# Optimization experiments

Measured on AMD Instinct MI355X. Metric: run time of the kernel, lower is better.

## Reference

```python
import jax, jax.numpy as jnp
import numpy as np


def setup_inputs() -> dict:
    key = jax.random.key(0)
    ks = jax.random.split(key, 11)
    B, T, I, H, O = 64, 256, 1024, 1024, 1024
    s_g = 1.0 / np.sqrt(I + H)  # torch Linear init scale (uniform); use scaled normal
    s_v = 1.0 / np.sqrt(H)
    return {
        "inputs": jax.random.normal(ks[0], (B, T, I), jnp.float32),
        "Wf_w": jax.random.normal(ks[1], (H, I + H), jnp.float32) * s_g,
        "Wf_b": jax.random.normal(ks[2], (H,), jnp.float32) * s_g,
        "Wi_w": jax.random.normal(ks[3], (H, I + H), jnp.float32) * s_g,
        "Wi_b": jax.random.normal(ks[4], (H,), jnp.float32) * s_g,
        "Wc_w": jax.random.normal(ks[5], (H, I + H), jnp.float32) * s_g,
        "Wc_b": jax.random.normal(ks[6], (H,), jnp.float32) * s_g,
        "Wo_w": jax.random.normal(ks[7], (H, I + H), jnp.float32) * s_g,
        "Wo_b": jax.random.normal(ks[8], (H,), jnp.float32) * s_g,
        "V_w": jax.random.normal(ks[9], (O, H), jnp.float32) * s_v,
        "V_b": jax.random.normal(ks[10], (O,), jnp.float32) * s_v,
    }


def reference(inputs, Wf_w, Wf_b, Wi_w, Wi_b, Wc_w, Wc_b, Wo_w, Wo_b, V_w, V_b):
    B, T, I = inputs.shape
    H = Wf_w.shape[0]
    # Fuse the four gate linears into one GEMM (mathematically identical).
    W_all = jnp.concatenate([Wf_w, Wi_w, Wo_w, Wc_w], axis=0)  # (4H, I+H)
    b_all = jnp.concatenate([Wf_b, Wi_b, Wo_b, Wc_b], axis=0)  # (4H,)

    def step(carry, x_t):  # x_t: (B, I)
        c, h = carry
        combined = jnp.concatenate([x_t, h], axis=1)            # (B, I+H)
        gates = combined @ W_all.T + b_all                      # (B, 4H)
        f, i, o, g = jnp.split(gates, 4, axis=1)
        f = jax.nn.sigmoid(f)
        i = jax.nn.sigmoid(i)
        o = jax.nn.sigmoid(o)
        g = jnp.tanh(g)
        c = f * c + i * g
        h = o * jnp.tanh(c)
        return (c, h), None

    c0 = jnp.zeros((B, H), inputs.dtype)
    h0 = jnp.zeros((B, H), inputs.dtype)
    (c, h), _ = jax.lax.scan(step, (c0, h0), jnp.swapaxes(inputs, 0, 1))
    last_out = h @ V_w.T + V_b  # outputs[:, -1, :] only depends on final h
    return (c, h, last_out)
```

## Files before the change

### kernel.cpp

```cpp
#include <hip/hip_runtime.h>
#include <hip/hip_bf16.h>

typedef __bf16 bf16x8 __attribute__((ext_vector_type(8)));
typedef float f32x4 __attribute__((ext_vector_type(4)));
typedef unsigned long long u64;

#define TSTEPS 256
#define NB 64
#define ID 1024
#define HD 1024
#define KD 2048

#define WOFF 0ull
#define VOFF 16777216ull
#define BOFF 18874368ull
#define HMOFF 18890752ull
#define XBOFF 52580352ull

#define SENT 0xFFFFFFFFu

__device__ __forceinline__ unsigned short f2b(float f) {
    unsigned int u = __float_as_uint(f);
    unsigned int r = (u + 0x7fffu + ((u >> 16) & 1u)) >> 16;
    return (unsigned short)r;
}

__device__ __forceinline__ bf16x8 as_frag(uint4 u) {
    union { uint4 u; bf16x8 v; } c; c.u = u; return c.v;
}

__device__ __forceinline__ uint4 ld_b128_cp(const void* p) {
    uint4 r;
    asm volatile("global_load_dwordx4 %0, %1, off sc0 sc1" : "=v"(r) : "v"(p));
    return r;
}
__device__ __forceinline__ uint4 ld_b128(const void* p) {
    uint4 r;
    asm volatile("global_load_dwordx4 %0, %1, off" : "=v"(r) : "v"(p));
    return r;
}

__global__ void cvt_x(const float* __restrict__ in, unsigned short* __restrict__ out) {
    size_t i = ((size_t)blockIdx.x * 256 + threadIdx.x) * 8;
    int t = (int)(i >> 16);
    int b = (int)(i >> 10) & 63;
    int k = (int)i & 1023;
    const float* src = in + ((size_t)b << 18) + ((size_t)t << 10) + k;
    float4 a = *(const float4*)src;
    float4 bb = *(const float4*)(src + 4);
    union { unsigned short h[8]; uint4 u; } o;
    o.h[0] = f2b(a.x); o.h[1] = f2b(a.y); o.h[2] = f2b(a.z); o.h[3] = f2b(a.w);
    o.h[4] = f2b(bb.x); o.h[5] = f2b(bb.y); o.h[6] = f2b(bb.z); o.h[7] = f2b(bb.w);
    *(uint4*)(out + i) = o.u;
}

__global__ void cvt_w(const float* __restrict__ Wf, const float* __restrict__ Wi,
                      const float* __restrict__ Wo, const float* __restrict__ Wc,
                      const float* __restrict__ bf_, const float* __restrict__ bi_,
                      const float* __restrict__ bo_, const float* __restrict__ bc_,
                      unsigned short* __restrict__ Wr, float* __restrict__ bias_r) {
    int idx = blockIdx.x * 256 + threadIdx.x;
    int np = idx >> 8;
    int k  = (idx & 255) * 8;
    int g = np & 3, h = np >> 2;
    const float* W = (g == 0) ? Wf : (g == 1) ? Wi : (g == 2) ? Wo : Wc;
    const float* src = W + (size_t)h * KD + k;
    float4 a = *(const float4*)src;
    float4 b = *(const float4*)(src + 4);
    union { unsigned short h[8]; uint4 u; } o;
    o.h[0] = f2b(a.x); o.h[1] = f2b(a.y); o.h[2] = f2b(a.z); o.h[3] = f2b(a.w);
    o.h[4] = f2b(b.x); o.h[5] = f2b(b.y); o.h[6] = f2b(b.z); o.h[7] = f2b(b.w);
    *(uint4*)(Wr + (size_t)np * KD + k) = o.u;
    if (k == 0) {
        const float* B = (g == 0) ? bf_ : (g == 1) ? bi_ : (g == 2) ? bo_ : bc_;
        bias_r[np] = B[h];
    }
}

__global__ void cvt_v(const float* __restrict__ V, unsigned short* __restrict__ out) {
    size_t i = ((size_t)blockIdx.x * blockDim.x + threadIdx.x) * 8;
    float4 a = *(const float4*)(V + i);
    float4 b = *(const float4*)(V + i + 4);
    union { unsigned short h[8]; uint4 u; } o;
    o.h[0] = f2b(a.x); o.h[1] = f2b(a.y); o.h[2] = f2b(a.z); o.h[3] = f2b(a.w);
    o.h[4] = f2b(b.x); o.h[5] = f2b(b.y); o.h[6] = f2b(b.z); o.h[7] = f2b(b.w);
    *(uint4*)(out + i) = o.u;
}

__global__ void init_h(unsigned short* __restrict__ h0) {
    size_t i = ((size_t)blockIdx.x * blockDim.x + threadIdx.x) * 8;
    uint4 z = {0, 0, 0, 0};
    *(uint4*)(h0 + i) = z;
}

__global__ void init_sent(unsigned short* __restrict__ h1) {
    size_t i = ((size_t)blockIdx.x * blockDim.x + threadIdx.x) * 8;
    uint4 s = {SENT, SENT, SENT, SENT};
    *(uint4*)(h1 + i) = s;
}

__device__ __forceinline__ float sigf(float x) {
    return 1.0f / (1.0f + __expf(-x));
}
__device__ __forceinline__ float tanhfast(float x) {
    return 2.0f / (1.0f + __expf(-2.0f * x)) - 1.0f;
}

__launch_bounds__(512, 1)
__global__ void lstm_core(const unsigned short* __restrict__ xb,
                          const unsigned short* __restrict__ Wr,
                          const float* __restrict__ bias_r,
                          unsigned short* __restrict__ hm,
                          const unsigned short* __restrict__ Vw,
                          const float* __restrict__ Vbias,
                          float* __restrict__ out) {
    __shared__ float gxp[8][64][20];

    const int bid  = blockIdx.x;
    const int tid  = threadIdx.x;
    const int wave = tid >> 6;
    const int lane = tid & 63;
    const int lrow = lane & 15;
    const int kq   = (lane >> 4) << 3;
    const int n0   = bid << 4;
    const int qr   = (lane >> 4) << 2;

    const int ct   = tid - 256;
    const int ob   = (ct >> 2) & 63;
    const int lhc  = ct & 3;
    const int hcol = (bid << 2) + lhc;
    float4 bb = {0, 0, 0, 0};
    if (tid >= 256) bb = *(const float4*)&bias_r[n0 + (lhc << 2)];

    const bool isx = wave < 4;
    const unsigned short* wptr = Wr + (size_t)(n0 + lrow) * KD + (wave << 8) + kq;

    uint4 wfrag[8];
    #pragma unroll
    for (int kk8 = 0; kk8 < 8; ++kk8)
        wfrag[kk8] = ld_b128(wptr + kk8 * 32);
    asm volatile("s_waitcnt vmcnt(0)" ::: "memory");
    __builtin_amdgcn_sched_barrier(0);

    int koff = 0;
    if (!isx) koff = ((wave - 4) << 8) + kq;
    const int xko = (wave << 8) + kq;

    float c_reg = 0.f;
    float hlast = 0.f;

    for (int t = 0; t < TSTEPS; ++t) {
        f32x4 acc[4];
        #pragma unroll
        for (int m = 0; m < 4; ++m) acc[m] = (f32x4){0, 0, 0, 0};

        if (isx) {
            const unsigned short* xt = xb + ((size_t)t << 16);
            #pragma unroll
            for (int kk8 = 0; kk8 < 8; ++kk8)
                #pragma unroll
                for (int m = 0; m < 4; ++m)
                    acc[m] = __builtin_amdgcn_mfma_f32_16x16x32_bf16(
                        *(const bf16x8*)(xt + (size_t)(m * 16 + lrow) * 1024 + xko + kk8 * 32),
                        as_frag(wfrag[kk8]), acc[m], 0, 0, 0);
        } else {
            const unsigned short* hmt = hm + ((size_t)t << 16);
            const int c8b = koff >> 3;
            uint4 hA[4][4], hB[4][4];

            int itA = 0;
            for (;;) {
                #pragma unroll
                for (int j = 0; j < 4; ++j)
                    #pragma unroll
                    for (int m = 0; m < 4; ++m)
                        hA[j][m] = ld_b128_cp(hmt + (size_t)(c8b + j * 4) * 512 + (m * 16 + lrow) * 8);
                asm volatile("s_waitcnt vmcnt(0)" ::: "memory");
                __builtin_amdgcn_sched_barrier(0);
                unsigned int bad = 0;
                #pragma unroll
                for (int j = 0; j < 4; ++j)
                    #pragma unroll
                    for (int m = 0; m < 4; ++m)
                        bad |= (hA[j][m].x == SENT) | (hA[j][m].y == SENT) |
                               (hA[j][m].z == SENT) | (hA[j][m].w == SENT);
                if (__all(bad == 0) || ++itA > (1 << 14)) break;
            }
            __builtin_amdgcn_sched_barrier(0);

            #pragma unroll
            for (int j = 0; j < 4; ++j)
                #pragma unroll
                for (int m = 0; m < 4; ++m)
                    hB[j][m] = ld_b128_cp(hmt + (size_t)(c8b + (j + 4) * 4) * 512 + (m * 16 + lrow) * 8);
            __builtin_amdgcn_sched_barrier(0);

            #pragma unroll
            for (int j = 0; j < 4; ++j)
                #pragma unroll
                for (int m = 0; m < 4; ++m)
                    acc[m] = __builtin_amdgcn_mfma_f32_16x16x32_bf16(as_frag(hA[j][m]),
                                                                     as_frag(wfrag[j]), acc[m], 0, 0, 0);

            int itB = 0;
            for (;;) {
                asm volatile("s_waitcnt vmcnt(0)" ::: "memory");
                __builtin_amdgcn_sched_barrier(0);
                unsigned int bad = 0;
                #pragma unroll
                for (int j = 0; j < 4; ++j)
                    #pragma unroll
                    for (int m = 0; m < 4; ++m)
                        bad |= (hB[j][m].x == SENT) | (hB[j][m].y == SENT) |
                               (hB[j][m].z == SENT) | (hB[j][m].w == SENT);
                if (__all(bad == 0) || ++itB > (1 << 14)) break;
                #pragma unroll
                for (int j = 0; j < 4; ++j)
                    #pragma unroll
                    for (int m = 0; m < 4; ++m)
                        hB[j][m] = ld_b128_cp(hmt + (size_t)(c8b + (j + 4) * 4) * 512 + (m * 16 + lrow) * 8);
            }
            __builtin_amdgcn_sched_barrier(0);

            #pragma unroll
            for (int j = 0; j < 4; ++j)
                #pragma unroll
                for (int m = 0; m < 4; ++m)
                    acc[m] = __builtin_amdgcn_mfma_f32_16x16x32_bf16(as_frag(hB[j][m]),
                                                                     as_frag(wfrag[j + 4]), acc[m], 0, 0, 0);
        }

        #pragma unroll
        for (int m = 0; m < 4; ++m)
            #pragma unroll
            for (int r = 0; r < 4; ++r)
                gxp[wave][m * 16 + qr + r][lrow] = acc[m][r];
        __syncthreads();

        if (tid >= 256) {
            float fpre = bb.x, ipre = bb.y, opre = bb.z, gpre = bb.w;
            #pragma unroll
            for (int w = 0; w < 8; ++w) {
                float4 s = *(const float4*)&gxp[w][ob][lhc << 2];
                fpre += s.x; ipre += s.y; opre += s.z; gpre += s.w;
            }
            float fg = sigf(fpre);
            float ig = sigf(ipre);
            float og = sigf(opre);
            float gg = tanhfast(gpre);
            c_reg = fg * c_reg + ig * gg;
            float hh = og * tanhfast(c_reg);
            if (t == TSTEPS - 1) hlast = hh;

            unsigned int hb = f2b(hh);
            unsigned int p1 = __shfl_down(hb, 1);
            unsigned int p2 = __shfl_down(hb, 2);
            unsigned int p3 = __shfl_down(hb, 3);
            if ((lane & 3) == 0) {
                u64 v = (u64)hb | ((u64)p1 << 16) | ((u64)p2 << 32) | ((u64)p3 << 48);
                unsigned short* dst = hm + ((size_t)(t + 1) << 16)
                                       + (size_t)(bid >> 1) * 512 + (size_t)ob * 8 + ((bid & 1) << 2);
                asm volatile("global_store_dwordx2 %0, %1, off sc0 sc1" :: "v"(dst), "v"(v) : "memory");
            }
        }
        __syncthreads();
    }

    if (tid >= 256) {
        out[(size_t)ob * HD + hcol] = c_reg;
        out[65536 + (size_t)ob * HD + hcol] = hlast;
    }

    if (bid < 64) {
        f32x4 acc[4];
        #pragma unroll
        for (int m = 0; m < 4; ++m) acc[m] = (f32x4){0, 0, 0, 0};
        const int ko2 = (wave << 7) + kq;
        const unsigned short* vp = Vw + (size_t)(n0 + lrow) * HD + ko2;
        const unsigned short* hmt = hm + ((size_t)TSTEPS << 16);
        const int c8b = ko2 >> 3;
        uint4 pw[4], pv[4][4];
        #pragma unroll
        for (int j = 0; j < 4; ++j)
            pw[j] = ld_b128(vp + j * 32);
        int it = 0;
        for (;;) {
            #pragma unroll
            for (int j = 0; j < 4; ++j)
                #pragma unroll
                for (int m = 0; m < 4; ++m)
                    pv[j][m] = ld_b128_cp(hmt + (size_t)(c8b + j * 4) * 512 + (m * 16 + lrow) * 8);
            asm volatile("s_waitcnt vmcnt(0)" ::: "memory");
            __builtin_amdgcn_sched_barrier(0);
            unsigned int bad = 0;
            #pragma unroll
            for (int j = 0; j < 4; ++j)
                #pragma unroll
                for (int m = 0; m < 4; ++m)
                    bad |= (pv[j][m].x == SENT) | (pv[j][m].y == SENT) |
                           (pv[j][m].z == SENT) | (pv[j][m].w == SENT);
            if (__all(bad == 0) || ++it > (1 << 14)) break;
        }
        __builtin_amdgcn_sched_barrier(0);
        #pragma unroll
        for (int j = 0; j < 4; ++j)
            #pragma unroll
            for (int m = 0; m < 4; ++m)
                acc[m] = __builtin_amdgcn_mfma_f32_16x16x32_bf16(as_frag(pv[j][m]),
                                                                 as_frag(pw[j]), acc[m], 0, 0, 0);
        #pragma unroll
        for (int m = 0; m < 4; ++m)
            #pragma unroll
            for (int r = 0; r < 4; ++r)
                gxp[wave][m * 16 + qr + r][lrow] = acc[m][r];
        __syncthreads();
        if (tid >= 256) {
            float4 vb = *(const float4*)&Vbias[n0 + (lhc << 2)];
            float4 res = vb;
            #pragma unroll
            for (int w = 0; w < 8; ++w) {
                float4 s = *(const float4*)&gxp[w][ob][lhc << 2];
                res.x += s.x; res.y += s.y; res.z += s.z; res.w += s.w;
            }
            *(float4*)&out[131072 + (size_t)ob * 1024 + n0 + (lhc << 2)] = res;
        }
    }
}

extern "C" void kernel_launch(void* const* d_in, const int* in_sizes, int n_in,
                              void* d_out, int out_size, void* d_ws, size_t ws_size,
                              hipStream_t stream) {
    const float* x   = (const float*)d_in[0];
    const float* Wf  = (const float*)d_in[1];
    const float* bf_ = (const float*)d_in[2];
    const float* Wi  = (const float*)d_in[3];
    const float* bi_ = (const float*)d_in[4];
    const float* Wc  = (const float*)d_in[5];
    const float* bc_ = (const float*)d_in[6];
    const float* Wo  = (const float*)d_in[7];
    const float* bo_ = (const float*)d_in[8];
    const float* Vw  = (const float*)d_in[9];
    const float* Vb  = (const float*)d_in[10];

    char* ws = (char*)d_ws;
    unsigned short* Wr     = (unsigned short*)(ws + WOFF);
    unsigned short* Vbf    = (unsigned short*)(ws + VOFF);
    float*          bias_r = (float*)(ws + BOFF);
    unsigned short* hm     = (unsigned short*)(ws + HMOFF);
    unsigned short* xbb    = (unsigned short*)(ws + XBOFF);
    float*          outp   = (float*)d_out;

    cvt_x <<<8192, 256, 0, stream>>>(x, xbb);
    cvt_w <<<4096, 256, 0, stream>>>(Wf, Wi, Wo, Wc, bf_, bi_, bo_, bc_, Wr, bias_r);
    cvt_v <<<512, 256, 0, stream>>>(Vw, Vbf);
    init_h<<<32, 256, 0, stream>>>(hm);
    init_sent<<<8192, 256, 0, stream>>>(hm + 65536);

    void* args[] = {&xbb, &Wr, &bias_r, &hm, &Vbf, (void*)&Vb, &outp};
    hipLaunchCooperativeKernel((const void*)lstm_core, dim3(256), dim3(512), args, 0, stream);
}
```

Baseline: 1.462 ms.

## Split waves by batch rows and precompute next-step input projection off critical path

Each of the 4 x-waves now computes the full-K input projection for its 16 batch rows one timestep ahead into a double-buffered shared array. Each of the 4 h-waves handles the full recurrent K for its 16 rows, streaming weights and hidden chunks with double buffering and per-chunk sentinel polling. The same wave then applies the gate nonlinearity, so the 8-wave cross reduction is gone and the t=0 recurrent GEMM and the h0 init kernel are skipped. In exchange, weights are reloaded from global or cache every step instead of being held in registers, which adds memory traffic.

```diff
diff --git a/kernel.cpp b/kernel.cpp
--- a/kernel.cpp
+++ b/kernel.cpp
@@ -87,12 +87,6 @@
     *(uint4*)(out + i) = o.u;
 }
 
-__global__ void init_h(unsigned short* __restrict__ h0) {
-    size_t i = ((size_t)blockIdx.x * blockDim.x + threadIdx.x) * 8;
-    uint4 z = {0, 0, 0, 0};
-    *(uint4*)(h0 + i) = z;
-}
-
 __global__ void init_sent(unsigned short* __restrict__ h1) {
     size_t i = ((size_t)blockIdx.x * blockDim.x + threadIdx.x) * 8;
     uint4 s = {SENT, SENT, SENT, SENT};
@@ -115,6 +109,8 @@
                           const float* __restrict__ Vbias,
                           float* __restrict__ out) {
     __shared__ float gxp[8][64][20];
+    __shared__ float pbx[4][2][16][20];
+    __shared__ float pbh[4][16][20];
 
     const int bid  = blockIdx.x;
     const int tid  = threadIdx.x;
@@ -125,125 +121,117 @@
     const int n0   = bid << 4;
     const int qr   = (lane >> 4) << 2;
 
+    const bool isx = wave < 4;
+    const int w4   = isx ? wave : wave - 4;
+    const int row0 = w4 << 4;
+    const int crow = lane >> 2;
+    const int chc  = lane & 3;
+
+    const unsigned short* wbase = Wr + (size_t)(n0 + lrow) * KD;
+    const float4 bb = *(const float4*)&bias_r[n0 + (chc << 2)];
+
     const int ct   = tid - 256;
     const int ob   = (ct >> 2) & 63;
     const int lhc  = ct & 3;
-    const int hcol = (bid << 2) + lhc;
-    float4 bb = {0, 0, 0, 0};
-    if (tid >= 256) bb = *(const float4*)&bias_r[n0 + (lhc << 2)];
-
-    const bool isx = wave < 4;
-    const unsigned short* wptr = Wr + (size_t)(n0 + lrow) * KD + (wave << 8) + kq;
-
-    uint4 wfrag[8];
-    #pragma unroll
-    for (int kk8 = 0; kk8 < 8; ++kk8)
-        wfrag[kk8] = ld_b128(wptr + kk8 * 32);
-    asm volatile("s_waitcnt vmcnt(0)" ::: "memory");
-    __builtin_amdgcn_sched_barrier(0);
-
-    int koff = 0;
-    if (!isx) koff = ((wave - 4) << 8) + kq;
-    const int xko = (wave << 8) + kq;
 
     float c_reg = 0.f;
     float hlast = 0.f;
 
+    if (isx) {
+        f32x4 acc = {0, 0, 0, 0};
+        const unsigned short* xrow = xb + (size_t)(row0 + lrow) * 1024 + kq;
+        #pragma unroll
+        for (int f = 0; f < 32; ++f)
+            acc = __builtin_amdgcn_mfma_f32_16x16x32_bf16(
+                *(const bf16x8*)(xrow + f * 32),
+                *(const bf16x8*)(wbase + f * 32 + kq), acc, 0, 0, 0);
+        #pragma unroll
+        for (int r = 0; r < 4; ++r) pbx[w4][0][qr + r][lrow] = acc[r];
+    }
+    __syncthreads();
+
     for (int t = 0; t < TSTEPS; ++t) {
-        f32x4 acc[4];
-        #pragma unroll
-        for (int m = 0; m < 4; ++m) acc[m] = (f32x4){0, 0, 0, 0};
-
         if (isx) {
-            const unsigned short* xt = xb + ((size_t)t << 16);
-            #pragma unroll
-            for (int kk8 = 0; kk8 < 8; ++kk8)
-                #pragma unroll
-                for (int m = 0; m < 4; ++m)
-                    acc[m] = __builtin_amdgcn_mfma_f32_16x16x32_bf16(
-                        *(const bf16x8*)(xt + (size_t)(m * 16 + lrow) * 1024 + xko + kk8 * 32),
-                        as_frag(wfrag[kk8]), acc[m], 0, 0, 0);
+            if (t + 1 < TSTEPS) {
+                f32x4 acc = {0, 0, 0, 0};
+                const unsigned short* xrow = xb + ((size_t)(t + 1) << 16)
+                                                + (size_t)(row0 + lrow) * 1024 + kq;
+                #pragma unroll
+                for (int f = 0; f < 32; ++f)
+                    acc = __builtin_amdgcn_mfma_f32_16x16x32_bf16(
+                        *(const bf16x8*)(xrow + f * 32),
+                        *(const bf16x8*)(wbase + f * 32 + kq), acc, 0, 0, 0);
+                #pragma unroll
+                for (int r = 0; r < 4; ++r) pbx[w4][(t + 1) & 1][qr + r][lrow] = acc[r];
+            }
         } else {
-            const unsigned short* hmt = hm + ((size_t)t << 16);
-            const int c8b = koff >> 3;
-            uint4 hA[4][4], hB[4][4];
-
-            int itA = 0;
-            for (;;) {
-                #pragma unroll
-                for (int j = 0; j < 4; ++j)
+            f32x4 acc = {0, 0, 0, 0};
+            if (t > 0) {
+                const unsigned short* hrow = hm + ((size_t)t << 16) + (size_t)(row0 + lrow) * 8;
+                uint4 hq[2][8], wq[2][8];
+                #pragma unroll
+                for (int f = 0; f < 8; ++f)
+                    wq[0][f] = ld_b128(wbase + 1024 + f * 32 + kq);
+                int it0 = 0;
+                for (;;) {
                     #pragma unroll
-                    for (int m = 0; m < 4; ++m)
-                        hA[j][m] = ld_b128_cp(hmt + (size_t)(c8b + j * 4) * 512 + (m * 16 + lrow) * 8);
-                asm volatile("s_waitcnt vmcnt(0)" ::: "memory");
+                    for (int f = 0; f < 8; ++f)
+                        hq[0][f] = ld_b128_cp(hrow + (size_t)(f * 4 + (lane >> 4)) * 512);
+                    asm volatile("s_waitcnt vmcnt(0)" ::: "memory");
+                    __builtin_amdgcn_sched_barrier(0);
+                    unsigned int bad = 0;
+                    #pragma unroll
+                    for (int f = 0; f < 8; ++f)
+                        bad |= (hq[0][f].x == SENT) | (hq[0][f].y == SENT) |
+                               (hq[0][f].z == SENT) | (hq[0][f].w == SENT);
+                    if (__all(bad == 0) || ++it0 > (1 << 15)) break;
+                }
                 __builtin_amdgcn_sched_barrier(0);
-                unsigned int bad = 0;
-                #pragma unroll
-                for (int j = 0; j < 4; ++j)
+                #pragma unroll
+                for (int q = 0; q < 4; ++q) {
+                    const int cur = q & 1, nxt = cur ^ 1;
+                    if (q < 3) {
+                        #pragma unroll
+                        for (int f = 0; f < 8; ++f) {
+                            wq[nxt][f] = ld_b128(wbase + 1024 + (q + 1) * 256 + f * 32 + kq);
+                            hq[nxt][f] = ld_b128_cp(hrow + (size_t)((q + 1) * 32 + f * 4 + (lane >> 4)) * 512);
+                        }
+                    }
                     #pragma unroll
-                    for (int m = 0; m < 4; ++m)
-                        bad |= (hA[j][m].x == SENT) | (hA[j][m].y == SENT) |
-                               (hA[j][m].z == SENT) | (hA[j][m].w == SENT);
-                if (__all(bad == 0) || ++itA > (1 << 14)) break;
+                    for (int f = 0; f < 8; ++f)
+                        acc = __builtin_amdgcn_mfma_f32_16x16x32_bf16(
+                            as_frag(hq[cur][f]), as_frag(wq[cur][f]), acc, 0, 0, 0);
+                    if (q < 3) {
+                        asm volatile("s_waitcnt vmcnt(0)" ::: "memory");
+                        __builtin_amdgcn_sched_barrier(0);
+                        int itq = 0;
+                        for (;;) {
+                            unsigned int bad = 0;
+                            #pragma unroll
+                            for (int f = 0; f < 8; ++f)
+                                bad |= (hq[nxt][f].x == SENT) | (hq[nxt][f].y == SENT) |
+                                       (hq[nxt][f].z == SENT) | (hq[nxt][f].w == SENT);
+                            if (__all(bad == 0) || ++itq > (1 << 15)) break;
+                            #pragma unroll
+                            for (int f = 0; f < 8; ++f)
+                                hq[nxt][f] = ld_b128_cp(hrow + (size_t)((q + 1) * 32 + f * 4 + (lane >> 4)) * 512);
+                            asm volatile("s_waitcnt vmcnt(0)" ::: "memory");
+                            __builtin_amdgcn_sched_barrier(0);
+                        }
+                        __builtin_amdgcn_sched_barrier(0);
+                    }
+                }
             }
+            #pragma unroll
+            for (int r = 0; r < 4; ++r) pbh[w4][qr + r][lrow] = acc[r];
+            asm volatile("s_waitcnt lgkmcnt(0)" ::: "memory");
             __builtin_amdgcn_sched_barrier(0);
-
-            #pragma unroll
-            for (int j = 0; j < 4; ++j)
-                #pragma unroll
-                for (int m = 0; m < 4; ++m)
-                    hB[j][m] = ld_b128_cp(hmt + (size_t)(c8b + (j + 4) * 4) * 512 + (m * 16 + lrow) * 8);
-            __builtin_amdgcn_sched_barrier(0);
-
-            #pragma unroll
-            for (int j = 0; j < 4; ++j)
-                #pragma unroll
-                for (int m = 0; m < 4; ++m)
-                    acc[m] = __builtin_amdgcn_mfma_f32_16x16x32_bf16(as_frag(hA[j][m]),
-                                                                     as_frag(wfrag[j]), acc[m], 0, 0, 0);
-
-            int itB = 0;
-            for (;;) {
-                asm volatile("s_waitcnt vmcnt(0)" ::: "memory");
-                __builtin_amdgcn_sched_barrier(0);
-                unsigned int bad = 0;
-                #pragma unroll
-                for (int j = 0; j < 4; ++j)
-                    #pragma unroll
-                    for (int m = 0; m < 4; ++m)
-                        bad |= (hB[j][m].x == SENT) | (hB[j][m].y == SENT) |
-                               (hB[j][m].z == SENT) | (hB[j][m].w == SENT);
-                if (__all(bad == 0) || ++itB > (1 << 14)) break;
-                #pragma unroll
-                for (int j = 0; j < 4; ++j)
-                    #pragma unroll
-                    for (int m = 0; m < 4; ++m)
-                        hB[j][m] = ld_b128_cp(hmt + (size_t)(c8b + (j + 4) * 4) * 512 + (m * 16 + lrow) * 8);
-            }
-            __builtin_amdgcn_sched_barrier(0);
-
-            #pragma unroll
-            for (int j = 0; j < 4; ++j)
-                #pragma unroll
-                for (int m = 0; m < 4; ++m)
-                    acc[m] = __builtin_amdgcn_mfma_f32_16x16x32_bf16(as_frag(hB[j][m]),
-                                                                     as_frag(wfrag[j + 4]), acc[m], 0, 0, 0);
-        }
-
-        #pragma unroll
-        for (int m = 0; m < 4; ++m)
-            #pragma unroll
-            for (int r = 0; r < 4; ++r)
-                gxp[wave][m * 16 + qr + r][lrow] = acc[m][r];
-        __syncthreads();
-
-        if (tid >= 256) {
-            float fpre = bb.x, ipre = bb.y, opre = bb.z, gpre = bb.w;
-            #pragma unroll
-            for (int w = 0; w < 8; ++w) {
-                float4 s = *(const float4*)&gxp[w][ob][lhc << 2];
-                fpre += s.x; ipre += s.y; opre += s.z; gpre += s.w;
-            }
+            float4 xp = *(const float4*)&pbx[w4][t & 1][crow][chc << 2];
+            float4 hp = *(const float4*)&pbh[w4][crow][chc << 2];
+            float fpre = xp.x + hp.x + bb.x;
+            float ipre = xp.y + hp.y + bb.y;
+            float opre = xp.z + hp.z + bb.z;
+            float gpre = xp.w + hp.w + bb.w;
             float fg = sigf(fpre);
             float ig = sigf(ipre);
             float og = sigf(opre);
@@ -256,19 +244,22 @@
             unsigned int p1 = __shfl_down(hb, 1);
             unsigned int p2 = __shfl_down(hb, 2);
             unsigned int p3 = __shfl_down(hb, 3);
-            if ((lane & 3) == 0) {
+            if (chc == 0) {
                 u64 v = (u64)hb | ((u64)p1 << 16) | ((u64)p2 << 32) | ((u64)p3 << 48);
                 unsigned short* dst = hm + ((size_t)(t + 1) << 16)
-                                       + (size_t)(bid >> 1) * 512 + (size_t)ob * 8 + ((bid & 1) << 2);
+                                       + (size_t)(bid >> 1) * 512
+                                       + (size_t)(row0 + crow) * 8 + ((bid & 1) << 2);
                 asm volatile("global_store_dwordx2 %0, %1, off sc0 sc1" :: "v"(dst), "v"(v) : "memory");
             }
         }
         __syncthreads();
     }
 
-    if (tid >= 256) {
-        out[(size_t)ob * HD + hcol] = c_reg;
-        out[65536 + (size_t)ob * HD + hcol] = hlast;
+    if (!isx) {
+        const int rg = row0 + crow;
+        const int cg = (bid << 2) + chc;
+        out[(size_t)rg * HD + cg] = c_reg;
+        out[65536 + (size_t)rg * HD + cg] = hlast;
     }
 
     if (bid < 64) {
@@ -353,7 +344,6 @@
     cvt_x <<<8192, 256, 0, stream>>>(x, xbb);
     cvt_w <<<4096, 256, 0, stream>>>(Wf, Wi, Wo, Wc, bf_, bi_, bo_, bc_, Wr, bias_r);
     cvt_v <<<512, 256, 0, stream>>>(Vw, Vbf);
-    init_h<<<32, 256, 0, stream>>>(hm);
     init_sent<<<8192, 256, 0, stream>>>(hm + 65536);
 
     void* args[] = {&xbb, &Wr, &bias_r, &hm, &Vbf, (void*)&Vb, &outp};
```

After: 3.360 ms. 2.3x slower.
